# Kernel optimization log

Measured on AMD Instinct MI355X. Metric: run time of the kernel, lower is better.

## Reference

```python
import jax, jax.numpy as jnp
import numpy as np

N_EVENTS = 8388608
H_DIM, W_DIM = 480, 640
BIN_WIDTH = 0.01
A_INIT = 1e-4  # initial a_x = a_y


def setup_inputs() -> dict:
    key = jax.random.key(0)
    k1, k2, k3, k4 = jax.random.split(key, 4)
    x = jax.random.uniform(k1, (N_EVENTS,), dtype=jnp.float32) * W_DIM
    y = jax.random.uniform(k2, (N_EVENTS,), dtype=jnp.float32) * H_DIM
    ts = jax.random.uniform(k3, (N_EVENTS,), dtype=jnp.float32)  # seconds in [0,1)
    pol = jnp.where(jax.random.bernoulli(k4, 0.5, (N_EVENTS,)), 1.0, -1.0).astype(jnp.float32)
    params = jnp.array([A_INIT, A_INIT], dtype=jnp.float32)
    # num_bins is data-dependent in the torch source (Python int from tensor min/max);
    # compute it here on concrete data so the jitted reference uses a static shape.
    t_w = ts - params[0] * x - params[1] * y
    num_bins = int((float(t_w.max()) - float(t_w.min())) / BIN_WIDTH) + 1
    return {
        'params': params,
        'x_coords': x, 'y_coords': y, 'timestamps': ts, 'polarities': pol,
        'H': H_DIM, 'W': W_DIM, 'bin_width': BIN_WIDTH, 'num_bins': num_bins,
    }


def _forward(params, x_coords, y_coords, timestamps, polarities, H, W, bin_width, num_bins):
    # warp: shift timestamps by learned scan parameters
    t_warped = timestamps - params[0] * x_coords - params[1] * y_coords
    t_start = t_warped.min()
    t_norm = (t_warped - t_start) / jnp.float32(bin_width)
    t0 = jnp.floor(t_norm)
    wt = t_norm - t0  # bilinear-in-time weight
    t0c = jnp.clip(t0, 0, num_bins - 1).astype(jnp.int32)
    t1c = jnp.clip(t0 + 1.0, 0, num_bins - 1).astype(jnp.int32)
    xi = x_coords.astype(jnp.int32)
    yi = y_coords.astype(jnp.int32)
    valid = (xi >= 0) & (xi < W) & (yi >= 0) & (yi < H)
    # masked-weight scatter == torch's boolean filtering before scatter_add
    vmask = valid.astype(jnp.float32)
    spatial = jnp.where(valid, yi * W + xi, 0)
    fi0 = t0c * (H * W) + spatial
    fi1 = t1c * (H * W) + spatial
    w0 = (1.0 - wt) * polarities * vmask
    w1 = wt * polarities * vmask
    num_elements = num_bins * H * W
    flat = jnp.zeros((num_elements,), dtype=jnp.float32)
    flat = flat.at[fi0].add(w0).at[fi1].add(w1)
    event_tensor = flat.reshape(num_bins, H, W)
    # torch.var is unbiased (ddof=1)
    variances = jnp.var(event_tensor.reshape(num_bins, -1), axis=1, ddof=1)
    loss = jnp.mean(variances)
    return event_tensor, loss


def reference(params, x_coords, y_coords, timestamps, polarities, H, W, bin_width, num_bins):
    return _forward(params, x_coords, y_coords, timestamps, polarities, H, W, bin_width, num_bins)
```

## Files before the change

### kernel.cpp

```cpp
#include <hip/hip_runtime.h>

#define W_ 640
#define H_ 480
#define HW_ (W_ * H_)
#define VAR_SPLIT 8
#define MAXNB_T 124
#define NBAND 120
#define NTX3 40
#define NT3 (NBAND * NTX3)
#define FB 48
#define FT 32
#define FB2 128
#define FT2 64
#define PAD 16
#define OVF 131072
#define CPB 8


__device__ __forceinline__ unsigned fkey(float f) {
    unsigned u = __float_as_uint(f);
    return (u & 0x80000000u) ? ~u : (u | 0x80000000u);
}
__device__ __forceinline__ float finv(unsigned k) {
    unsigned u = (k & 0x80000000u) ? (k ^ 0x80000000u) : ~k;
    return __uint_as_float(u);
}
__device__ __forceinline__ float warp_t(float ts, float xf, float yf, float p0, float p1) {
    return __fsub_rn(__fsub_rn(ts, __fmul_rn(p0, xf)), __fmul_rn(p1, yf));
}

__device__ __forceinline__ void spill_rec(unsigned r, int band,
                                          int* ovfcur, uint2* ovfrecs) {
    int j = atomicAdd(ovfcur, 1);
    if (j < OVF) {
        int pix = (int)((r >> 12) & 63u);
        int yi = band * 4 + (pix >> 4);
        int xi = (int)((r >> 18) & 63u) * 16 + (pix & 15);
        int b = (int)((r >> 24) & 127u);
        float wt = __fmul_rn((float)(r & 4095u), 2.44140625e-4f);
        unsigned px = ((unsigned)b << 20) | (unsigned)(yi * W_ + xi) | (r & 0x80000000u);
        ovfrecs[j] = make_uint2(px, __float_as_uint(wt));
    }
}

__global__ void k_init(float* __restrict__ out, int n4, unsigned* __restrict__ minbits,
                       int* __restrict__ ovfcur, double* __restrict__ sums, int nsums,
                       int* __restrict__ curs, int ncur) {
    int tid = blockIdx.x * blockDim.x + threadIdx.x;
    int stride = gridDim.x * blockDim.x;
    float4* o4 = (float4*)out;
    float4 z = make_float4(0.f, 0.f, 0.f, 0.f);
    for (int i = tid; i < n4; i += stride) o4[i] = z;
    for (int i = tid; i < ncur; i += stride) curs[i] = 0;
    if (tid == 0) { *minbits = 0xFFFFFFFFu; *ovfcur = 0; }
    if (tid < nsums) sums[tid] = 0.0;
}

__global__ void k_min(const float* __restrict__ x, const float* __restrict__ y,
                      const float* __restrict__ ts, const float* __restrict__ params,
                      int n, unsigned* __restrict__ minbits) {
    float p0 = params[0], p1 = params[1];
    int tid = blockIdx.x * blockDim.x + threadIdx.x;
    int stride = gridDim.x * blockDim.x;
    int n4 = n >> 2;
    const float4* x4 = (const float4*)x;
    const float4* y4 = (const float4*)y;
    const float4* t4 = (const float4*)ts;
    unsigned k = 0xFFFFFFFFu;
    for (int i = tid; i < n4; i += stride) {
        float4 xv = x4[i], yv = y4[i], tv = t4[i];
        unsigned k0 = fkey(warp_t(tv.x, xv.x, yv.x, p0, p1));
        unsigned k1 = fkey(warp_t(tv.y, xv.y, yv.y, p0, p1));
        unsigned k2 = fkey(warp_t(tv.z, xv.z, yv.z, p0, p1));
        unsigned k3 = fkey(warp_t(tv.w, xv.w, yv.w, p0, p1));
        unsigned ka = min(k0, k1), kb = min(k2, k3);
        k = min(k, min(ka, kb));
    }
    for (int i = (n4 << 2) + tid; i < n; i += stride)
        k = min(k, fkey(warp_t(ts[i], x[i], y[i], p0, p1)));
    #pragma unroll
    for (int off = 32; off > 0; off >>= 1) {
        unsigned o = __shfl_down(k, off, 64);
        k = (o < k) ? o : k;
    }
    if ((threadIdx.x & 63) == 0) atomicMin(minbits, k);
}

__global__ void __launch_bounds__(256) k_pass1(
        const float* __restrict__ x, const float* __restrict__ y,
        const float* __restrict__ ts, const float* __restrict__ pol,
        const float* __restrict__ params, const float* __restrict__ bwp,
        int n, int nb, int cap1, int per, const unsigned* __restrict__ minbits,
        int* __restrict__ gcur, unsigned* __restrict__ recs1,
        int* __restrict__ ovfcur, uint2* __restrict__ ovfrecs) {
    __shared__ unsigned buf[NBAND][FB];
    __shared__ int cnt[NBAND];
    float p0 = params[0], p1 = params[1], bw = bwp[0];
    float tstart = finv(*minbits);
    float nbm1 = (float)(nb - 1);
    for (int t = threadIdx.x; t < NBAND; t += 256) cnt[t] = 0;
    __syncthreads();
    int lo = blockIdx.x * per;
    int hi = min(n, lo + per);
    int total = (hi > lo) ? (hi - lo) : 0;
    int nf4 = total >> 2;
    const float4* x4 = (const float4*)(x + lo);
    const float4* y4 = (const float4*)(y + lo);
    const float4* t4 = (const float4*)(ts + lo);
    const float4* p4 = (const float4*)(pol + lo);
    int wave = threadIdx.x >> 6, lane = threadIdx.x & 63;

    auto proc = [&](float xf, float yf, float tf, float pf) {
        int xi = (int)xf, yi = (int)yf;
        if (xi >= 0 && xi < W_ && yi >= 0 && yi < H_) {
            float tn = __fdiv_rn(__fsub_rn(warp_t(tf, xf, yf, p0, p1), tstart), bw);
            float t0f = floorf(tn);
            float wt = __fsub_rn(tn, t0f);
            int b = (int)fminf(fmaxf(t0f, 0.0f), nbm1);
            unsigned sgn = __float_as_uint(pf) & 0x80000000u;
            int band = yi >> 2;
            unsigned tilex = (unsigned)(xi >> 4);
            unsigned pix = (unsigned)(((yi & 3) << 4) | (xi & 15));
            unsigned wq = (unsigned)__fmul_rn(wt, 4096.0f);
            unsigned rec = sgn | ((unsigned)b << 24) | (tilex << 18) | (pix << 12) | wq;
            int pos = atomicAdd(&cnt[band], 1);
            if (pos < FB) buf[band][pos] = rec;
            else {
                int j = atomicAdd(ovfcur, 1);
                if (j < OVF) {
                    unsigned px = ((unsigned)b << 20) | (unsigned)(yi * W_ + xi) | sgn;
                    ovfrecs[j] = make_uint2(px, __float_as_uint(wt));
                }
            }
        }
    };
    auto flush = [&](int thresh) {
        for (int bb = wave; bb < NBAND; bb += 4) {
            int c = min(cnt[bb], FB);
            if (c >= thresh) {
                int base = 0;
                if (lane == 0) base = atomicAdd(&gcur[bb * PAD], c);
                base = __shfl(base, 0, 64);
                for (int j = lane; j < c; j += 64) {
                    unsigned r = buf[bb][j];
                    int idx = base + j;
                    if (idx < cap1) recs1[(size_t)bb * cap1 + idx] = r;
                    else spill_rec(r, bb, ovfcur, ovfrecs);
                }
                if (lane == 0) cnt[bb] = 0;
            }
        }
    };

    int iters = (nf4 + 255) >> 8;
    for (int it = 0; it < iters; it++) {
        int i4 = (it << 8) + (int)threadIdx.x;
        bool valid = (i4 < nf4);
        float4 xv, yv, tv, pv;
        if (valid) { xv = x4[i4]; yv = y4[i4]; tv = t4[i4]; pv = p4[i4]; }
        if (valid) {
            proc(xv.x, yv.x, tv.x, pv.x);
            proc(xv.y, yv.y, tv.y, pv.y);
            proc(xv.z, yv.z, tv.z, pv.z);
            proc(xv.w, yv.w, tv.w, pv.w);
        }
        __syncthreads();
        flush(FT);
        __syncthreads();
    }
    int tbase = lo + (nf4 << 2);
    int trem = hi - tbase;
    if ((int)threadIdx.x < trem) {
        int i = tbase + (int)threadIdx.x;
        proc(x[i], y[i], ts[i], pol[i]);
    }
    __syncthreads();
    flush(1);
}

__global__ void __launch_bounds__(256) k_pass2(
        const unsigned* __restrict__ recs1, const int* __restrict__ gcur,
        int cap1, int cap2, int* __restrict__ tcur, unsigned* __restrict__ recs2,
        int* __restrict__ ovfcur, uint2* __restrict__ ovfrecs) {
    __shared__ unsigned buf[NTX3][FB2];
    __shared__ int cnt[NTX3];
    int band = blockIdx.x / CPB;
    int chunk = blockIdx.x % CPB;
    int c1 = min(gcur[band * PAD], cap1);
    int chunklen = (((c1 + CPB - 1) / CPB) + 3) & ~3;
    int start = chunk * chunklen;
    int end = min(start + chunklen, c1);
    const unsigned* seg = recs1 + (size_t)band * cap1;
    for (int t = threadIdx.x; t < NTX3; t += 256) cnt[t] = 0;
    __syncthreads();
    int iters = (end > start) ? ((end - start + 1023) >> 10) : 0;
    int wave = threadIdx.x >> 6, lane = threadIdx.x & 63;
    for (int it = 0; it < iters; it++) {
        int idx = start + (it << 10) + (int)threadIdx.x * 4;
        unsigned r4[4];
        int m = 0;
        if (idx + 4 <= end) {
            uint4 q = *(const uint4*)&seg[idx];
            r4[0] = q.x; r4[1] = q.y; r4[2] = q.z; r4[3] = q.w; m = 4;
        } else {
            for (; idx + m < end && m < 4; m++) r4[m] = seg[idx + m];
        }
        #pragma unroll
        for (int k = 0; k < 4; k++) {
            if (k < m) {
                unsigned r = r4[k];
                int tx = min((int)((r >> 18) & 63u), NTX3 - 1);
                int pos = atomicAdd(&cnt[tx], 1);
                if (pos < FB2) buf[tx][pos] = r;
                else spill_rec(r, band, ovfcur, ovfrecs);
            }
        }
        __syncthreads();
        bool last = (it == iters - 1);
        for (int bb = wave; bb < NTX3; bb += 4) {
            int c = min(cnt[bb], FB2);
            if (c >= (last ? 1 : FT2)) {
                int base = 0;
                if (lane == 0) base = atomicAdd(&tcur[(band * NTX3 + bb) * PAD], c);
                base = __shfl(base, 0, 64);
                for (int j = lane; j < c; j += 64) {
                    unsigned r = buf[bb][j];
                    int o = base + j;
                    if (o < cap2) recs2[(size_t)(band * NTX3 + bb) * cap2 + o] = r;
                    else spill_rec(r, band, ovfcur, ovfrecs);
                }
                if (lane == 0) cnt[bb] = 0;
            }
        }
        __syncthreads();
    }
}

__global__ void __launch_bounds__(256) k_accum6(
        const unsigned* __restrict__ recs2, const int* __restrict__ tcur,
        int nb, int cap2, float* __restrict__ out, double2* __restrict__ part2) {
    extern __shared__ float acc[];
    int T = blockIdx.x;
    int ry = T / NTX3, tx = T % NTX3;
    int nacc4 = nb << 4;
    float4* acc4 = (float4*)acc;
    float4 z4 = make_float4(0.f, 0.f, 0.f, 0.f);
    for (int i = threadIdx.x; i < nacc4; i += 256) acc4[i] = z4;
    __syncthreads();
    int c2 = min(tcur[T * PAD], cap2);
    const unsigned* seg = recs2 + (size_t)T * cap2;
    int iters = (c2 + 1023) >> 10;
    for (int it = 0; it < iters; it++) {
        int idx = (it << 10) + (int)threadIdx.x * 4;
        unsigned r4[4];
        int m = 0;
        if (idx + 4 <= c2) {
            uint4 q = *(const uint4*)&seg[idx];
            r4[0] = q.x; r4[1] = q.y; r4[2] = q.z; r4[3] = q.w; m = 4;
        } else {
            for (; idx + m < c2 && m < 4; m++) r4[m] = seg[idx + m];
        }
        #pragma unroll
        for (int k = 0; k < 4; k++) {
            if (k < m) {
                unsigned r = r4[k];
                int b = min((int)((r >> 24) & 127u), nb - 1);
                int b1 = min(b + 1, nb - 1);
                int pix = (int)((r >> 12) & 63u);
                unsigned sgn = r & 0x80000000u;
                float wt = __fmul_rn((float)(r & 4095u), 2.44140625e-4f);
                float w0 = __uint_as_float(__float_as_uint(__fsub_rn(1.0f, wt)) ^ sgn);
                float w1 = __uint_as_float(__float_as_uint(wt) ^ sgn);
                atomicAdd(&acc[(b << 6) + pix], w0);
                atomicAdd(&acc[(b1 << 6) + pix], w1);
            }
        }
    }
    __syncthreads();
    int x0 = tx * 16, y0 = ry * 4;
    for (int i = threadIdx.x; i < nacc4; i += 256) {
        int b = i >> 4;
        int q = i & 15;
        int row = q >> 2, qx = q & 3;
        *(float4*)&out[(size_t)b * HW_ + (size_t)(y0 + row) * W_ + x0 + (qx << 2)] = acc4[i];
    }
    int t = threadIdx.x;
    if (t < 2 * nb) {
        int b = t >> 1, half = t & 1;
        double s = 0.0, ss = 0.0;
        int basei = (b << 6) + (half << 5);
        for (int jj = 0; jj < 32; jj++) {
            float v = acc[basei + ((jj + b) & 31)];
            double dv = (double)v;
            s += dv; ss += dv * dv;
        }
        part2[(size_t)t * NT3 + T] = make_double2(s, ss);
    }
}

__global__ void __launch_bounds__(256) k_redsum(
        const double2* __restrict__ part2, int nb,
        double* __restrict__ sumv, double* __restrict__ sumsq) {
    int b = blockIdx.x;
    const double2* r0 = part2 + (size_t)(2 * b) * NT3;
    const double2* r1 = part2 + (size_t)(2 * b + 1) * NT3;
    double s = 0.0, ss = 0.0;
    for (int i = threadIdx.x; i < NT3; i += 256) {
        double2 a = r0[i];
        double2 c = r1[i];
        s += a.x + c.x; ss += a.y + c.y;
    }
    #pragma unroll
    for (int off = 32; off > 0; off >>= 1) {
        s += __shfl_down(s, off, 64);
        ss += __shfl_down(ss, off, 64);
    }
    __shared__ double sb[4], sb2[4];
    int wave = threadIdx.x >> 6, lane = threadIdx.x & 63;
    if (lane == 0) { sb[wave] = s; sb2[wave] = ss; }
    __syncthreads();
    if (threadIdx.x == 0) {
        for (int i = 1; i < 4; i++) { s += sb[i]; ss += sb2[i]; }
        sumv[b] = s; sumsq[b] = ss;
    }
}

__global__ void __launch_bounds__(256) k_accum2(
        const unsigned* __restrict__ recs1, const int* __restrict__ gcur,
        int nb, int cap1, float* __restrict__ out,
        double* __restrict__ sumv, double* __restrict__ sumsq) {
    extern __shared__ float acc[];
    int h = blockIdx.x;
    int xcd = h & 7;
    int j = h >> 3;
    int kk2 = j / NTX3;
    int tx = j % NTX3;
    int ry = xcd + 8 * kk2;
    int nacc = nb << 6;
    for (int i = threadIdx.x; i < nacc; i += 256) acc[i] = 0.f;
    __syncthreads();
    int c1 = min(gcur[ry * PAD], cap1);
    const unsigned* seg = recs1 + (size_t)ry * cap1;
    unsigned txu = (unsigned)tx;
    int iters = (c1 + 1023) >> 10;
    for (int it = 0; it < iters; it++) {
        int idx = (it << 10) + (int)threadIdx.x * 4;
        unsigned r4[4];
        int m = 0;
        if (idx + 4 <= c1) {
            uint4 q = *(const uint4*)&seg[idx];
            r4[0] = q.x; r4[1] = q.y; r4[2] = q.z; r4[3] = q.w; m = 4;
        } else {
            for (; idx + m < c1 && m < 4; m++) r4[m] = seg[idx + m];
        }
        #pragma unroll
        for (int k = 0; k < 4; k++) {
            if (k < m) {
                unsigned r = r4[k];
                if (((r >> 18) & 63u) == txu) {
                    int b = min((int)((r >> 24) & 127u), nb - 1);
                    int b1 = min(b + 1, nb - 1);
                    int pix = (int)((r >> 12) & 63u);
                    unsigned sgn = r & 0x80000000u;
                    float wt = __fmul_rn((float)(r & 4095u), 2.44140625e-4f);
                    float w0 = __uint_as_float(__float_as_uint(__fsub_rn(1.0f, wt)) ^ sgn);
                    float w1 = __uint_as_float(__float_as_uint(wt) ^ sgn);
                    atomicAdd(&acc[(b << 6) + pix], w0);
                    atomicAdd(&acc[(b1 << 6) + pix], w1);
                }
            }
        }
    }
    __syncthreads();
    int x0 = tx * 16, y0 = ry * 4;
    for (int i = threadIdx.x; i < nacc; i += 256) {
        int b = i >> 6, p = i & 63;
        int yy = y0 + (p >> 4), xx = x0 + (p & 15);
        out[(size_t)b * HW_ + yy * W_ + xx] = acc[i];
    }
    if ((int)threadIdx.x < nb) {
        int b = threadIdx.x;
        double s = 0.0, ss = 0.0;
        for (int j2 = 0; j2 < 64; j2++) {
            float v = acc[(b << 6) + ((j2 + b) & 63)];
            double dv = (double)v;
            s += dv; ss += dv * dv;
        }
        atomicAdd(&sumv[b], s);
        atomicAdd(&sumsq[b], ss);
    }
}

__global__ void k_ovf(const uint2* __restrict__ ovfrecs, const int* __restrict__ ovfcur,
                      int nb, float* __restrict__ out,
                      double* __restrict__ sumv, double* __restrict__ sumsq) {
    int m = min(*ovfcur, OVF);
    int tid = blockIdx.x * blockDim.x + threadIdx.x;
    int stride = gridDim.x * blockDim.x;
    for (int i = tid; i < m; i += stride) {
        uint2 r = ovfrecs[i];
        unsigned sgn = r.x & 0x80000000u;
        int b = (int)((r.x >> 20) & 511u);
        int sp = (int)(r.x & 0x7FFFFu);
        b = min(b, nb - 1); sp = min(sp, HW_ - 1);
        int b1 = min(b + 1, nb - 1);
        float wt = __uint_as_float(r.y);
        float w0 = __uint_as_float(__float_as_uint(__fsub_rn(1.0f, wt)) ^ sgn);
        float w1 = __uint_as_float(r.y ^ sgn);
        float o0 = unsafeAtomicAdd(out + (size_t)b * HW_ + sp, w0);
        atomicAdd(&sumv[b], (double)w0);
        atomicAdd(&sumsq[b], (double)w0 * ((double)w0 + 2.0 * (double)o0));
        float o1 = unsafeAtomicAdd(out + (size_t)b1 * HW_ + sp, w1);
        atomicAdd(&sumv[b1], (double)w1);
        atomicAdd(&sumsq[b1], (double)w1 * ((double)w1 + 2.0 * (double)o1));
    }
}

__global__ void k_scatter(const float* __restrict__ x, const float* __restrict__ y,
                          const float* __restrict__ ts, const float* __restrict__ pol,
                          const float* __restrict__ params, const float* __restrict__ bwp,
                          int n, int nb, const unsigned* __restrict__ minbits,
                          float* __restrict__ out) {
    float p0 = params[0], p1 = params[1];
    float bw = bwp[0];
    float tstart = finv(*minbits);
    float nbm1 = (float)(nb - 1);
    int tid = blockIdx.x * blockDim.x + threadIdx.x;
    int stride = gridDim.x * blockDim.x;
    for (int i = tid; i < n; i += stride) {
        float xf = x[i], yf = y[i];
        float tn = __fdiv_rn(__fsub_rn(warp_t(ts[i], xf, yf, p0, p1), tstart), bw);
        float t0f = floorf(tn);
        float wt = __fsub_rn(tn, t0f);
        int t0c = (int)fminf(fmaxf(t0f, 0.0f), nbm1);
        int t1c = (int)fminf(fmaxf(__fadd_rn(t0f, 1.0f), 0.0f), nbm1);
        int xi = (int)xf, yi = (int)yf;
        if (xi >= 0 && xi < W_ && yi >= 0 && yi < H_) {
            int sp = yi * W_ + xi;
            float p = pol[i];
            float w0 = __fmul_rn(__fsub_rn(1.0f, wt), p);
            float w1 = __fmul_rn(wt, p);
            unsafeAtomicAdd(&out[(size_t)t0c * HW_ + sp], w0);
            unsafeAtomicAdd(&out[(size_t)t1c * HW_ + sp], w1);
        }
    }
}

__global__ void k_sums(const float* __restrict__ out, double* __restrict__ sumv,
                       double* __restrict__ sumsq) {
    int b = blockIdx.x / VAR_SPLIT;
    int part = blockIdx.x % VAR_SPLIT;
    const int chunk = HW_ / VAR_SPLIT;
    const float* p = out + (size_t)b * HW_ + (size_t)part * chunk;
    double s = 0.0, ss = 0.0;
    for (int i = threadIdx.x; i < chunk; i += blockDim.x) {
        double v = (double)p[i];
        s += v; ss += v * v;
    }
    #pragma unroll
    for (int off = 32; off > 0; off >>= 1) {
        s += __shfl_down(s, off, 64);
        ss += __shfl_down(ss, off, 64);
    }
    __shared__ double sb[8], sb2[8];
    int wave = threadIdx.x >> 6, lane = threadIdx.x & 63;
    if (lane == 0) { sb[wave] = s; sb2[wave] = ss; }
    __syncthreads();
    if (threadIdx.x == 0) {
        int nw = blockDim.x >> 6;
        for (int i = 1; i < nw; i++) { s += sb[i]; ss += sb2[i]; }
        atomicAdd(&sumv[b], s);
        atomicAdd(&sumsq[b], ss);
    }
}

__global__ void k_final(const double* __restrict__ sumv, const double* __restrict__ sumsq,
                        int nb, float* __restrict__ loss) {
    double acc = 0.0;
    const double n = (double)HW_;
    for (int b = threadIdx.x; b < nb; b += blockDim.x) {
        double s = sumv[b], ss = sumsq[b];
        acc += (ss - s * s / n) / (n - 1.0);
    }
    #pragma unroll
    for (int off = 32; off > 0; off >>= 1) acc += __shfl_down(acc, off, 64);
    __shared__ double sb[8];
    int wave = threadIdx.x >> 6, lane = threadIdx.x & 63;
    if (lane == 0) sb[wave] = acc;
    __syncthreads();
    if (threadIdx.x == 0) {
        int nw = blockDim.x >> 6;
        for (int i = 1; i < nw; i++) acc += sb[i];
        *loss = (float)(acc / (double)nb);
    }
}

extern "C" void kernel_launch(void* const* d_in, const int* in_sizes, int n_in,
                              void* d_out, int out_size, void* d_ws, size_t ws_size,
                              hipStream_t stream) {
    const float* params = (const float*)d_in[0];
    const float* x      = (const float*)d_in[1];
    const float* y      = (const float*)d_in[2];
    const float* ts     = (const float*)d_in[3];
    const float* pol    = (const float*)d_in[4];
    const float* bwp    = (const float*)d_in[7];

    int n  = in_sizes[1];
    int nb = (out_size - 1) / HW_;
    float* out = (float*)d_out;

    size_t off_sums  = 128;
    size_t off_gcur  = (off_sums + 16ULL * nb + 63) & ~(size_t)63;
    size_t off_tcur  = off_gcur + 4ULL * NBAND * PAD;
    size_t off_part  = (off_tcur + 4ULL * NT3 * PAD + 63) & ~(size_t)63;
    size_t off_ovfr  = (off_part + 16ULL * 2 * nb * NT3 + 63) & ~(size_t)63;
    size_t off_recs1 = (off_ovfr + 8ULL * OVF + 63) & ~(size_t)63;

    unsigned* minbits = (unsigned*)d_ws;
    int*      ovfcur  = (int*)((char*)d_ws + 64);
    double*   sumv    = (double*)((char*)d_ws + off_sums);
    double*   sumsq   = sumv + nb;
    int*      gcur    = (int*)((char*)d_ws + off_gcur);
    int*      tcur    = (int*)((char*)d_ws + off_tcur);
    double2*  part2   = (double2*)((char*)d_ws + off_part);
    uint2*    ovfrecs = (uint2*)((char*)d_ws + off_ovfr);
    unsigned* recs1   = (unsigned*)((char*)d_ws + off_recs1);

    long long mean1 = (long long)n / NBAND;
    long long mean2 = (long long)n / NT3;

    long long cap1e = (mean1 + mean1 / 8 + 2048) & ~3LL;
    size_t off_recs2 = (off_recs1 + 4ULL * NBAND * cap1e + 63) & ~(size_t)63;
    unsigned* recs2 = (unsigned*)((char*)d_ws + off_recs2);
    long long avail2 = (ws_size > off_recs2)
                       ? (long long)((ws_size - off_recs2) / (4ULL * NT3)) : 0;
    long long cap2min = mean2 + mean2 / 8 + 128;
    long long cap2max = 2 * mean2 + 512;
    long long cap2ll = ((avail2 < cap2max) ? avail2 : cap2max) & ~3LL;
    bool exact = (n > 0) && (nb >= 1) && (nb <= MAXNB_T) && (cap2ll >= cap2min);

    long long avail1 = (ws_size > off_recs1)
                       ? (long long)((ws_size - off_recs1) / (4ULL * NBAND)) : 0;
    long long cap1f_max = 2 * mean1 + 4096;
    long long cap1fll = ((avail1 < cap1f_max) ? avail1 : cap1f_max) & ~3LL;
    bool filter = !exact && (n > 0) && (nb >= 1) && (nb <= MAXNB_T) &&
                  (cap1fll >= mean1 + mean1 / 12 + 2048);

    int cap1 = (int)(exact ? cap1e : cap1fll);
    int cap2 = (int)cap2ll;

    int n_tensor = nb * HW_;
    int n4 = (exact || filter) ? 0 : (n_tensor >> 2);

    const int BLK = 256;
    const int G1 = 1280;
    const int ITBLK = 1024;
    int per = (((n + G1 - 1) / G1) + ITBLK - 1) / ITBLK * ITBLK;
    int g1used = (n + per - 1) / per;

    hipLaunchKernelGGL(k_init, dim3(2048), dim3(BLK), 0, stream,
                       out, n4, minbits, ovfcur, sumv, 2 * nb,
                       gcur, NBAND * PAD + NT3 * PAD);
    hipLaunchKernelGGL(k_min, dim3(2048), dim3(BLK), 0, stream,
                       x, y, ts, params, n, minbits);

    if (exact) {
        hipLaunchKernelGGL(k_pass1, dim3(g1used), dim3(BLK), 0, stream,
                           x, y, ts, pol, params, bwp, n, nb, cap1, per, minbits,
                           gcur, recs1, ovfcur, ovfrecs);
        hipLaunchKernelGGL(k_pass2, dim3(NBAND * CPB), dim3(BLK), 0, stream,
                           recs1, gcur, cap1, cap2, tcur, recs2, ovfcur, ovfrecs);
        hipLaunchKernelGGL(k_accum6, dim3(NT3), dim3(BLK), (size_t)nb * 64 * 4, stream,
                           recs2, tcur, nb, cap2, out, part2);
        hipLaunchKernelGGL(k_redsum, dim3(nb), dim3(BLK), 0, stream,
                           part2, nb, sumv, sumsq);
        hipLaunchKernelGGL(k_ovf, dim3(64), dim3(BLK), 0, stream,
                           ovfrecs, ovfcur, nb, out, sumv, sumsq);
    } else if (filter) {
        hipLaunchKernelGGL(k_pass1, dim3(g1used), dim3(BLK), 0, stream,
                           x, y, ts, pol, params, bwp, n, nb, cap1, per, minbits,
                           gcur, recs1, ovfcur, ovfrecs);
        hipLaunchKernelGGL(k_accum2, dim3(NT3), dim3(BLK), (size_t)nb * 64 * 4, stream,
                           recs1, gcur, nb, cap1, out, sumv, sumsq);
        hipLaunchKernelGGL(k_ovf, dim3(64), dim3(BLK), 0, stream,
                           ovfrecs, ovfcur, nb, out, sumv, sumsq);
    } else {
        hipLaunchKernelGGL(k_scatter, dim3(2048), dim3(BLK), 0, stream,
                           x, y, ts, pol, params, bwp, n, nb, minbits, out);
        hipLaunchKernelGGL(k_sums, dim3(nb * VAR_SPLIT), dim3(BLK), 0, stream,
                           out, sumv, sumsq);
    }

    hipLaunchKernelGGL(k_final, dim3(1), dim3(BLK), 0, stream,
                       sumv, sumsq, nb, out + n_tensor);
}
```

Measured before the change: 368.4 us.

## Use 64-wide single-row tiles, double per-iteration batching, and transpose partial-sum layout

Spatial tiles in the two-level binning change from 16x4 pixel blocks to 1x64 row segments. Each bin's accumulator then writes to one contiguous 256-byte span of the output row, which should give more coalesced stores. Pass 1 and pass 2 now load two vector groups per iteration before each flush barrier, which halves the number of syncthreads, and ITBLK is doubled to match. The per-tile partial sums are stored tile-major, and the init grid is shrunk. The extra loads raise register pressure, and each flush now drains a fuller shared buffer, which may cause more overflow spills.

```diff
diff --git a/kernel.cpp b/kernel.cpp
--- a/kernel.cpp
+++ b/kernel.cpp
@@ -6,8 +6,8 @@
 #define VAR_SPLIT 8
 #define MAXNB_T 124
 #define NBAND 120
-#define NTX3 40
-#define NT3 (NBAND * NTX3)
+#define NTK 40
+#define NT3 (NBAND * NTK)
 #define FB 48
 #define FT 32
 #define FB2 128
@@ -33,9 +33,10 @@
                                           int* ovfcur, uint2* ovfrecs) {
     int j = atomicAdd(ovfcur, 1);
     if (j < OVF) {
+        int tk = min((int)((r >> 18) & 63u), NTK - 1);
         int pix = (int)((r >> 12) & 63u);
-        int yi = band * 4 + (pix >> 4);
-        int xi = (int)((r >> 18) & 63u) * 16 + (pix & 15);
+        int yi = band * 4 + tk / 10;
+        int xi = (tk % 10) * 64 + pix;
         int b = (int)((r >> 24) & 127u);
         float wt = __fmul_rn((float)(r & 4095u), 2.44140625e-4f);
         unsigned px = ((unsigned)b << 20) | (unsigned)(yi * W_ + xi) | (r & 0x80000000u);
@@ -119,10 +120,10 @@
             int b = (int)fminf(fmaxf(t0f, 0.0f), nbm1);
             unsigned sgn = __float_as_uint(pf) & 0x80000000u;
             int band = yi >> 2;
-            unsigned tilex = (unsigned)(xi >> 4);
-            unsigned pix = (unsigned)(((yi & 3) << 4) | (xi & 15));
+            unsigned tk = (unsigned)((yi & 3) * 10 + (xi >> 6));
+            unsigned pix = (unsigned)(xi & 63);
             unsigned wq = (unsigned)__fmul_rn(wt, 4096.0f);
-            unsigned rec = sgn | ((unsigned)b << 24) | (tilex << 18) | (pix << 12) | wq;
+            unsigned rec = sgn | ((unsigned)b << 24) | (tk << 18) | (pix << 12) | wq;
             int pos = atomicAdd(&cnt[band], 1);
             if (pos < FB) buf[band][pos] = rec;
             else {
@@ -152,17 +153,26 @@
         }
     };
 
-    int iters = (nf4 + 255) >> 8;
+    int iters = (nf4 + 511) >> 9;
     for (int it = 0; it < iters; it++) {
-        int i4 = (it << 8) + (int)threadIdx.x;
-        bool valid = (i4 < nf4);
-        float4 xv, yv, tv, pv;
-        if (valid) { xv = x4[i4]; yv = y4[i4]; tv = t4[i4]; pv = p4[i4]; }
-        if (valid) {
-            proc(xv.x, yv.x, tv.x, pv.x);
-            proc(xv.y, yv.y, tv.y, pv.y);
-            proc(xv.z, yv.z, tv.z, pv.z);
-            proc(xv.w, yv.w, tv.w, pv.w);
+        int base4 = it << 9;
+        int ia = base4 + (int)threadIdx.x;
+        int ib = ia + 256;
+        bool va = (ia < nf4), vb = (ib < nf4);
+        float4 xa, ya, ta, pa, xb, yb, tb, pb;
+        if (va) { xa = x4[ia]; ya = y4[ia]; ta = t4[ia]; pa = p4[ia]; }
+        if (vb) { xb = x4[ib]; yb = y4[ib]; tb = t4[ib]; pb = p4[ib]; }
+        if (va) {
+            proc(xa.x, ya.x, ta.x, pa.x);
+            proc(xa.y, ya.y, ta.y, pa.y);
+            proc(xa.z, ya.z, ta.z, pa.z);
+            proc(xa.w, ya.w, ta.w, pa.w);
+        }
+        if (vb) {
+            proc(xb.x, yb.x, tb.x, pb.x);
+            proc(xb.y, yb.y, tb.y, pb.y);
+            proc(xb.z, yb.z, tb.z, pb.z);
+            proc(xb.w, yb.w, tb.w, pb.w);
         }
         __syncthreads();
         flush(FT);
@@ -182,8 +192,8 @@
         const unsigned* __restrict__ recs1, const int* __restrict__ gcur,
         int cap1, int cap2, int* __restrict__ tcur, unsigned* __restrict__ recs2,
         int* __restrict__ ovfcur, uint2* __restrict__ ovfrecs) {
-    __shared__ unsigned buf[NTX3][FB2];
-    __shared__ int cnt[NTX3];
+    __shared__ unsigned buf[NTK][FB2];
+    __shared__ int cnt[NTK];
     int band = blockIdx.x / CPB;
     int chunk = blockIdx.x % CPB;
     int c1 = min(gcur[band * PAD], cap1);
@@ -191,13 +201,11 @@
     int start = chunk * chunklen;
     int end = min(start + chunklen, c1);
     const unsigned* seg = recs1 + (size_t)band * cap1;
-    for (int t = threadIdx.x; t < NTX3; t += 256) cnt[t] = 0;
-    __syncthreads();
-    int iters = (end > start) ? ((end - start + 1023) >> 10) : 0;
+    for (int t = threadIdx.x; t < NTK; t += 256) cnt[t] = 0;
+    __syncthreads();
     int wave = threadIdx.x >> 6, lane = threadIdx.x & 63;
-    for (int it = 0; it < iters; it++) {
-        int idx = start + (it << 10) + (int)threadIdx.x * 4;
-        unsigned r4[4];
+
+    auto load4 = [&](int idx, unsigned* r4) -> int {
         int m = 0;
         if (idx + 4 <= end) {
             uint4 q = *(const uint4*)&seg[idx];
@@ -205,28 +213,38 @@
         } else {
             for (; idx + m < end && m < 4; m++) r4[m] = seg[idx + m];
         }
+        return m;
+    };
+    auto place = [&](unsigned r) {
+        int tx = min((int)((r >> 18) & 63u), NTK - 1);
+        int pos = atomicAdd(&cnt[tx], 1);
+        if (pos < FB2) buf[tx][pos] = r;
+        else spill_rec(r, band, ovfcur, ovfrecs);
+    };
+
+    int iters = (end > start) ? ((end - start + 2047) >> 11) : 0;
+    for (int it = 0; it < iters; it++) {
+        int i1 = start + (it << 11) + (int)threadIdx.x * 4;
+        int i2 = i1 + 1024;
+        unsigned ra[4], rb[4];
+        int ma = load4(i1, ra);
+        int mb = load4(i2, rb);
         #pragma unroll
-        for (int k = 0; k < 4; k++) {
-            if (k < m) {
-                unsigned r = r4[k];
-                int tx = min((int)((r >> 18) & 63u), NTX3 - 1);
-                int pos = atomicAdd(&cnt[tx], 1);
-                if (pos < FB2) buf[tx][pos] = r;
-                else spill_rec(r, band, ovfcur, ovfrecs);
-            }
-        }
+        for (int k = 0; k < 4; k++) if (k < ma) place(ra[k]);
+        #pragma unroll
+        for (int k = 0; k < 4; k++) if (k < mb) place(rb[k]);
         __syncthreads();
         bool last = (it == iters - 1);
-        for (int bb = wave; bb < NTX3; bb += 4) {
+        for (int bb = wave; bb < NTK; bb += 4) {
             int c = min(cnt[bb], FB2);
             if (c >= (last ? 1 : FT2)) {
                 int base = 0;
-                if (lane == 0) base = atomicAdd(&tcur[(band * NTX3 + bb) * PAD], c);
+                if (lane == 0) base = atomicAdd(&tcur[(band * NTK + bb) * PAD], c);
                 base = __shfl(base, 0, 64);
                 for (int j = lane; j < c; j += 64) {
                     unsigned r = buf[bb][j];
                     int o = base + j;
-                    if (o < cap2) recs2[(size_t)(band * NTX3 + bb) * cap2 + o] = r;
+                    if (o < cap2) recs2[(size_t)(band * NTK + bb) * cap2 + o] = r;
                     else spill_rec(r, band, ovfcur, ovfrecs);
                 }
                 if (lane == 0) cnt[bb] = 0;
@@ -241,7 +259,9 @@
         int nb, int cap2, float* __restrict__ out, double2* __restrict__ part2) {
     extern __shared__ float acc[];
     int T = blockIdx.x;
-    int ry = T / NTX3, tx = T % NTX3;
+    int band = T / NTK, tk = T % NTK;
+    int yy = band * 4 + tk / 10;
+    int x0 = (tk % 10) * 64;
     int nacc4 = nb << 4;
     float4* acc4 = (float4*)acc;
     float4 z4 = make_float4(0.f, 0.f, 0.f, 0.f);
@@ -277,12 +297,11 @@
         }
     }
     __syncthreads();
-    int x0 = tx * 16, y0 = ry * 4;
+    size_t rowbase = (size_t)yy * W_ + x0;
     for (int i = threadIdx.x; i < nacc4; i += 256) {
         int b = i >> 4;
         int q = i & 15;
-        int row = q >> 2, qx = q & 3;
-        *(float4*)&out[(size_t)b * HW_ + (size_t)(y0 + row) * W_ + x0 + (qx << 2)] = acc4[i];
+        *(float4*)&out[(size_t)b * HW_ + rowbase + (q << 2)] = acc4[i];
     }
     int t = threadIdx.x;
     if (t < 2 * nb) {
@@ -294,7 +313,7 @@
             double dv = (double)v;
             s += dv; ss += dv * dv;
         }
-        part2[(size_t)t * NT3 + T] = make_double2(s, ss);
+        part2[(size_t)T * (2 * nb) + t] = make_double2(s, ss);
     }
 }
 
@@ -302,12 +321,10 @@
         const double2* __restrict__ part2, int nb,
         double* __restrict__ sumv, double* __restrict__ sumsq) {
     int b = blockIdx.x;
-    const double2* r0 = part2 + (size_t)(2 * b) * NT3;
-    const double2* r1 = part2 + (size_t)(2 * b + 1) * NT3;
     double s = 0.0, ss = 0.0;
     for (int i = threadIdx.x; i < NT3; i += 256) {
-        double2 a = r0[i];
-        double2 c = r1[i];
+        double2 a = part2[(size_t)i * (2 * nb) + 2 * b];
+        double2 c = part2[(size_t)i * (2 * nb) + 2 * b + 1];
         s += a.x + c.x; ss += a.y + c.y;
     }
     #pragma unroll
@@ -333,15 +350,15 @@
     int h = blockIdx.x;
     int xcd = h & 7;
     int j = h >> 3;
-    int kk2 = j / NTX3;
-    int tx = j % NTX3;
+    int kk2 = j / NTK;
+    int tk = j % NTK;
     int ry = xcd + 8 * kk2;
     int nacc = nb << 6;
     for (int i = threadIdx.x; i < nacc; i += 256) acc[i] = 0.f;
     __syncthreads();
     int c1 = min(gcur[ry * PAD], cap1);
     const unsigned* seg = recs1 + (size_t)ry * cap1;
-    unsigned txu = (unsigned)tx;
+    unsigned tku = (unsigned)tk;
     int iters = (c1 + 1023) >> 10;
     for (int it = 0; it < iters; it++) {
         int idx = (it << 10) + (int)threadIdx.x * 4;
@@ -357,7 +374,7 @@
         for (int k = 0; k < 4; k++) {
             if (k < m) {
                 unsigned r = r4[k];
-                if (((r >> 18) & 63u) == txu) {
+                if (((r >> 18) & 63u) == tku) {
                     int b = min((int)((r >> 24) & 127u), nb - 1);
                     int b1 = min(b + 1, nb - 1);
                     int pix = (int)((r >> 12) & 63u);
@@ -372,11 +389,11 @@
         }
     }
     __syncthreads();
-    int x0 = tx * 16, y0 = ry * 4;
+    int yy = ry * 4 + tk / 10;
+    int x0 = (tk % 10) * 64;
     for (int i = threadIdx.x; i < nacc; i += 256) {
         int b = i >> 6, p = i & 63;
-        int yy = y0 + (p >> 4), xx = x0 + (p & 15);
-        out[(size_t)b * HW_ + yy * W_ + xx] = acc[i];
+        out[(size_t)b * HW_ + (size_t)yy * W_ + x0 + p] = acc[i];
     }
     if ((int)threadIdx.x < nb) {
         int b = threadIdx.x;
@@ -554,11 +571,11 @@
 
     const int BLK = 256;
     const int G1 = 1280;
-    const int ITBLK = 1024;
+    const int ITBLK = 2048;
     int per = (((n + G1 - 1) / G1) + ITBLK - 1) / ITBLK * ITBLK;
     int g1used = (n + per - 1) / per;
 
-    hipLaunchKernelGGL(k_init, dim3(2048), dim3(BLK), 0, stream,
+    hipLaunchKernelGGL(k_init, dim3(512), dim3(BLK), 0, stream,
                        out, n4, minbits, ovfcur, sumv, 2 * nb,
                        gcur, NBAND * PAD + NT3 * PAD);
     hipLaunchKernelGGL(k_min, dim3(2048), dim3(BLK), 0, stream,
```

After: 525.7 us. 42.7% more time.
